# Optimization experiments

Hardware: AMD Instinct MI355X
Metric: run time of the kernel (lower is better)

The kernel has to match this reference:

```python
import jax, jax.numpy as jnp
import numpy as np

N, M = 2048, 16384          # rows = target points, cols = density-map pixels
SIGMA = 0.1                 # entropic regularization
TOL = 5e-4                  # 5 * 0.0001 convergence threshold from the source
MAX_ITERS = 100
EPS = 1e-7


def setup_inputs() -> dict:
    key = jax.random.key(0)
    k1, k2, k3 = jax.random.split(key, 3)
    dis_mtx_cross = jax.random.uniform(k1, (N, M), dtype=jnp.float32)
    pre_density = jax.random.uniform(k2, (M,), dtype=jnp.float32)
    target_mass = jax.random.uniform(k3, (N,), dtype=jnp.float32)
    return {
        "dis_mtx_cross": dis_mtx_cross,
        "pre_density": pre_density,
        "target_mass": target_mass,
    }


def _c_transform(pow_dis, alpha):
    # -log( sum_i alpha_i * exp(-pow_dis[i, :]) + eps ), reduce over dim 0
    s = jnp.sum(jnp.exp(-pow_dis) * alpha[:, None], axis=0)
    return -jnp.log(s + EPS)


def reference(dis_mtx_cross, pre_density, target_mass):
    D = dis_mtx_cross / SIGMA  # done once in __init__ in the original
    n, m = D.shape

    def step(carry, _):
        g, f, done = carry
        # one Sinkhorn c-transform sweep (runs at least once, as in torch)
        f_new = _c_transform(D - g[:, None], target_mass) / (1.0 + SIGMA)
        g_new = _c_transform(D.T - f_new[:, None], pre_density)
        diff = SIGMA * jnp.mean(jnp.abs(g_new - g))
        # freeze state once converged (emulates the torch `break`)
        g_out = jnp.where(done, g, g_new)
        f_out = jnp.where(done, f, f_new)
        done = done | (diff < TOL)
        return (g_out, f_out, done), None

    g0 = jnp.zeros((n,), jnp.float32)
    f0 = jnp.zeros((m,), jnp.float32)
    (g, f, _), _ = jax.lax.scan(step, (g0, f0, jnp.array(False)), None,
                                length=MAX_ITERS)
    g = g * SIGMA
    f = 1.0 - jnp.exp(-f * SIGMA)
    return f, g
```

## Files before the change

kernel.cpp:

```cpp
#include <hip/hip_runtime.h>
#include <math.h>

#define NN 2048
#define MM 16384

typedef __attribute__((ext_vector_type(4))) float f32x4;
typedef __attribute__((ext_vector_type(2))) float f32x2;


__global__ __launch_bounds__(256)
void k_prep(const float* __restrict__ D,
            unsigned char* __restrict__ K8,
            unsigned char* __restrict__ KT8) {
    __shared__ unsigned char t[64][72];
    const int j0 = blockIdx.x * 64, i0 = blockIdx.y * 64;
    const int tid = threadIdx.x;
    const int r = tid >> 4, c4 = tid & 15;
#pragma unroll
    for (int rp = 0; rp < 4; ++rp) {
        const int row = i0 + rp * 16 + r;
        f32x4 d = *(const f32x4*)(D + (size_t)row * MM + j0 + c4 * 4);
        float e0 = __expf(-10.0f * d[0]);
        float e1 = __expf(-10.0f * d[1]);
        float e2 = __expf(-10.0f * d[2]);
        float e3 = __expf(-10.0f * d[3]);
        int p = __builtin_amdgcn_cvt_pk_fp8_f32(e0, e1, 0, false);
        p = __builtin_amdgcn_cvt_pk_fp8_f32(e2, e3, p, true);
        *(unsigned*)(K8 + (size_t)row * MM + j0 + c4 * 4) = (unsigned)p;
        t[c4 * 4 + 0][rp * 16 + r] = (unsigned char)(p & 0xff);
        t[c4 * 4 + 1][rp * 16 + r] = (unsigned char)((p >> 8) & 0xff);
        t[c4 * 4 + 2][rp * 16 + r] = (unsigned char)((p >> 16) & 0xff);
        t[c4 * 4 + 3][rp * 16 + r] = (unsigned char)((p >> 24) & 0xff);
    }
    __syncthreads();
#pragma unroll
    for (int p2 = 0; p2 < 4; ++p2) {
        const int item = p2 * 256 + tid;
        const int jl = item >> 4, iw = item & 15;
        unsigned val = *(const unsigned*)&t[jl][iw * 4];
        *(unsigned*)(KT8 + (size_t)(j0 + jl) * NN + i0 + iw * 4) = val;
    }
}

__global__ void k_init(const float* __restrict__ tm,
                       float* __restrict__ g, float* __restrict__ w,
                       unsigned* __restrict__ counter, int* __restrict__ done) {
    const int i = blockIdx.x * 256 + threadIdx.x;
    if (i < NN) { g[i] = 0.0f; w[i] = tm[i]; }
    if (i == 0) { *counter = 0u; *done = 0; }
}

__global__ __launch_bounds__(256, 2)
void k_phaseA(const unsigned char* __restrict__ KT8, const float* __restrict__ pd,
              const float* __restrict__ w, float* __restrict__ f,
              float* __restrict__ v, const int* __restrict__ done) {
    if (*done) return;
    const int tid = threadIdx.x, lane = tid & 63, wid = tid >> 6;

    float wr[2][16];
#pragma unroll
    for (int k = 0; k < 2; ++k) {
        const f32x4* p = (const f32x4*)(w + k * 1024 + lane * 16);
#pragma unroll
        for (int q = 0; q < 4; ++q) {
            f32x4 a = p[q];
            wr[k][q * 4 + 0] = a[0]; wr[k][q * 4 + 1] = a[1];
            wr[k][q * 4 + 2] = a[2]; wr[k][q * 4 + 3] = a[3];
        }
    }
    const int jbase = blockIdx.x * 16 + wid * 4;
#pragma unroll
    for (int r = 0; r < 4; ++r) {
        const int j = jbase + r;
        const unsigned char* row = KT8 + (size_t)j * NN;
        float acc = 0.0f;
#pragma unroll
        for (int k = 0; k < 2; ++k) {
            uint4 qw = *(const uint4*)(row + k * 1024 + lane * 16);
            unsigned u[4] = {qw.x, qw.y, qw.z, qw.w};
#pragma unroll
            for (int c = 0; c < 4; ++c) {
                f32x2 lo = __builtin_amdgcn_cvt_pk_f32_fp8(u[c], false);
                f32x2 hi = __builtin_amdgcn_cvt_pk_f32_fp8(u[c], true);
                acc = fmaf(lo[0], wr[k][c * 4 + 0], acc);
                acc = fmaf(lo[1], wr[k][c * 4 + 1], acc);
                acc = fmaf(hi[0], wr[k][c * 4 + 2], acc);
                acc = fmaf(hi[1], wr[k][c * 4 + 3], acc);
            }
        }
#pragma unroll
        for (int s = 32; s; s >>= 1) acc += __shfl_xor(acc, s, 64);
        if (lane == 0) {
            float fj = -__logf(acc + 1e-7f) * (1.0f / 1.1f);
            f[j] = fj;
            v[j] = pd[j] * __expf(fj);
        }
    }
}

__global__ __launch_bounds__(256, 2)
void k_phaseB(const unsigned char* __restrict__ K8, const float* __restrict__ tm,
              const float* __restrict__ v, float* __restrict__ g,
              float* __restrict__ w, float* __restrict__ diffpart,
              unsigned* __restrict__ counter, int* __restrict__ done) {
    if (*done) return;
    const int tid = threadIdx.x;
    const int i0  = blockIdx.x * 4;

    float vr[4][16];
#pragma unroll
    for (int k = 0; k < 4; ++k) {
        const f32x4* p = (const f32x4*)(v + k * 4096 + tid * 16);
#pragma unroll
        for (int q = 0; q < 4; ++q) {
            f32x4 a = p[q];
            vr[k][q * 4 + 0] = a[0]; vr[k][q * 4 + 1] = a[1];
            vr[k][q * 4 + 2] = a[2]; vr[k][q * 4 + 3] = a[3];
        }
    }
    f32x4 accv = {0.f, 0.f, 0.f, 0.f};
#pragma unroll
    for (int r = 0; r < 4; ++r) {
        const unsigned char* row = K8 + (size_t)(i0 + r) * MM;
        float acc = 0.0f;
#pragma unroll
        for (int k = 0; k < 4; ++k) {
            uint4 qw = *(const uint4*)(row + k * 4096 + tid * 16);
            unsigned u[4] = {qw.x, qw.y, qw.z, qw.w};
#pragma unroll
            for (int c = 0; c < 4; ++c) {
                f32x2 lo = __builtin_amdgcn_cvt_pk_f32_fp8(u[c], false);
                f32x2 hi = __builtin_amdgcn_cvt_pk_f32_fp8(u[c], true);
                acc = fmaf(lo[0], vr[k][c * 4 + 0], acc);
                acc = fmaf(lo[1], vr[k][c * 4 + 1], acc);
                acc = fmaf(hi[0], vr[k][c * 4 + 2], acc);
                acc = fmaf(hi[1], vr[k][c * 4 + 3], acc);
            }
        }
        accv[r] = acc;
    }
    __shared__ f32x4 red[256];
    red[tid] = accv;
    __syncthreads();
    for (int s = 128; s; s >>= 1) {
        if (tid < s) red[tid] += red[tid + s];
        __syncthreads();
    }
    __shared__ bool last;
    if (tid == 0) {
        f32x4 sv = red[0];
        float dp = 0.0f;
#pragma unroll
        for (int r = 0; r < 4; ++r) {
            float gn = -__logf(sv[r] + 1e-7f);
            dp += fabsf(gn - g[i0 + r]);
            g[i0 + r] = gn;
            w[i0 + r] = tm[i0 + r] * __expf(gn);
        }
        diffpart[blockIdx.x] = dp;
        __threadfence();
        unsigned old = atomicAdd(counter, 1u);
        last = (old == gridDim.x - 1);
    }
    __syncthreads();

    if (last) {
        __threadfence();
        __shared__ float red1[256];
        red1[tid] = diffpart[tid] + diffpart[tid + 256];
        __syncthreads();
        for (int s2 = 128; s2; s2 >>= 1) {
            if (tid < s2) red1[tid] += red1[tid + s2];
            __syncthreads();
        }
        if (tid == 0) {
            if (0.1f * (red1[0] / (float)NN) < 5e-4f) *done = 1;
            *counter = 0u;
        }
    }
}

__global__ void k_out(const float* __restrict__ f,
                      const float* __restrict__ g,
                      float* __restrict__ out) {
    const int idx = blockIdx.x * 256 + threadIdx.x;
    if (idx < MM) {
        out[idx] = 1.0f - __expf(-0.1f * f[idx]);
    } else if (idx < MM + NN) {
        out[idx] = 0.1f * g[idx - MM];
    }
}

__global__ void k_f_partial(const float* __restrict__ dis,
                            const float* __restrict__ tm,
                            const float* __restrict__ g,
                            float* __restrict__ s_f,
                            const int* __restrict__ done) {
    if (*done) return;
    const int j  = blockIdx.x * 256 + threadIdx.x;
    const int i0 = blockIdx.y * (NN / 8);
    const float* p = dis + (size_t)i0 * MM + j;
    float acc = 0.f;
#pragma unroll 4
    for (int i = 0; i < NN / 8; ++i) {
        float d = p[(size_t)i * MM];
        float e = __expf(fmaf(d, -10.0f, g[i0 + i]));
        acc = fmaf(tm[i0 + i], e, acc);
    }
    atomicAdd(&s_f[j], acc);
}

__global__ void k_f_final(float* __restrict__ f, float* __restrict__ s_f,
                          const int* __restrict__ done) {
    if (*done) return;
    const int j = blockIdx.x * 256 + threadIdx.x;
    f[j] = -__logf(s_f[j] + 1e-7f) * (1.0f / 1.1f);
    s_f[j] = 0.f;
}

__global__ void k_g_row(const float* __restrict__ dis,
                        const float* __restrict__ pd,
                        const float* __restrict__ f,
                        float* __restrict__ g,
                        float* __restrict__ diff_acc,
                        const int* __restrict__ done) {
    if (*done) return;
    const int i = blockIdx.x;
    const float* p = dis + (size_t)i * MM;
    float acc = 0.f;
#pragma unroll 4
    for (int j = threadIdx.x; j < MM; j += 256) {
        float e = __expf(fmaf(p[j], -10.0f, f[j]));
        acc = fmaf(pd[j], e, acc);
    }
    __shared__ float red[256];
    red[threadIdx.x] = acc;
    __syncthreads();
    for (int s = 128; s > 0; s >>= 1) {
        if (threadIdx.x < s) red[threadIdx.x] += red[threadIdx.x + s];
        __syncthreads();
    }
    if (threadIdx.x == 0) {
        float gn = -__logf(red[0] + 1e-7f);
        atomicAdd(diff_acc, fabsf(gn - g[i]));
        g[i] = gn;
    }
}

__global__ void k_check(float* __restrict__ diff_acc, int* __restrict__ done) {
    if (!*done) {
        float diff = 0.1f * (*diff_acc / (float)NN);
        if (diff < 5e-4f) *done = 1;
    }
    *diff_acc = 0.f;
}

extern "C" void kernel_launch(void* const* d_in, const int* in_sizes, int n_in,
                              void* d_out, int out_size, void* d_ws, size_t ws_size,
                              hipStream_t stream) {
    const float* dis = (const float*)d_in[0];
    const float* pd  = (const float*)d_in[1];
    const float* tm  = (const float*)d_in[2];
    float* out = (float*)d_out;

    const size_t kBytes = (size_t)NN * MM;
    const size_t need   = 2 * kBytes
                        + (size_t)(2 * MM + 3 * NN + 512) * sizeof(float) + 64;

    if (ws_size >= need) {
        unsigned char* K8  = (unsigned char*)d_ws;
        unsigned char* KT8 = (unsigned char*)d_ws + kBytes;
        float* fbuf     = (float*)((char*)d_ws + 2 * kBytes);
        float* vbuf     = fbuf + MM;
        float* gbuf     = vbuf + MM;
        float* wbuf     = gbuf + NN;
        float* diffpart = wbuf + NN;
        unsigned* counter = (unsigned*)(diffpart + 512);
        int*      done    = (int*)(counter + 1);

        k_init<<<(NN + 255) / 256, 256, 0, stream>>>(tm, gbuf, wbuf, counter, done);
        k_prep<<<dim3(MM / 64, NN / 64), 256, 0, stream>>>(dis, K8, KT8);

        for (int it = 0; it < 100; ++it) {
            k_phaseA<<<1024, 256, 0, stream>>>(KT8, pd, wbuf, fbuf, vbuf, done);
            k_phaseB<<<512, 256, 0, stream>>>(K8, tm, vbuf, gbuf, wbuf,
                                              diffpart, counter, done);
        }
        k_out<<<(MM + NN + 255) / 256, 256, 0, stream>>>(fbuf, gbuf, out);
    } else {
        float* g        = (float*)d_ws;
        float* f        = g + NN;
        float* s_f      = f + MM;
        float* diff_acc = s_f + MM;
        int*   done     = (int*)(diff_acc + 1);

        hipMemsetAsync(d_ws, 0, (size_t)(NN + 2 * MM + 2) * sizeof(float), stream);

        dim3 gridF(MM / 256, 8);
        for (int it = 0; it < 100; ++it) {
            k_f_partial<<<gridF, 256, 0, stream>>>(dis, tm, g, s_f, done);
            k_f_final<<<MM / 256, 256, 0, stream>>>(f, s_f, done);
            k_g_row<<<NN, 256, 0, stream>>>(dis, pd, f, g, diff_acc, done);
            k_check<<<1, 1, 0, stream>>>(diff_acc, done);
        }
        k_out<<<(MM + NN + 255) / 256, 256, 0, stream>>>(f, g, out);
    }
}
```

Measured before the change: 909.6 us.

## Fuse Sinkhorn phases into one kernel with in-kernel grid barrier

Merges the two per-iteration kernels into a single kernel of 512 blocks. Each block computes 32 columns of f, then joins a global atomic-counter barrier before computing its rows of g. The init kernel is folded into the prep kernel. This halves the kernel launches and their gaps per iteration. In exchange it relies on all 512 blocks being co-resident, which launch_bounds(256,2) is meant to guarantee; if they are not, the spin barrier can deadlock. Phase A work per block doubles.

After: 2.106 ms. 2.32x slower.

```diff
diff --git a/kernel.cpp b/kernel.cpp
--- a/kernel.cpp
+++ b/kernel.cpp
@@ -3,15 +3,27 @@
 
 #define NN 2048
 #define MM 16384
+#define NB 512
 
 typedef __attribute__((ext_vector_type(4))) float f32x4;
 typedef __attribute__((ext_vector_type(2))) float f32x2;
+
+struct Bar { unsigned cntA; unsigned cntB; int flagA; int done; };
 
 
 __global__ __launch_bounds__(256)
 void k_prep(const float* __restrict__ D,
             unsigned char* __restrict__ K8,
-            unsigned char* __restrict__ KT8) {
+            unsigned char* __restrict__ KT8,
+            const float* __restrict__ tm,
+            float* __restrict__ g, float* __restrict__ w,
+            Bar* __restrict__ bar) {
+    if (blockIdx.x == 0 && blockIdx.y == 0) {
+        for (int i = threadIdx.x; i < NN; i += 256) { g[i] = 0.0f; w[i] = tm[i]; }
+        if (threadIdx.x == 0) {
+            bar->cntA = 0u; bar->cntB = 0u; bar->flagA = 0; bar->done = 0;
+        }
+    }
     __shared__ unsigned char t[64][72];
     const int j0 = blockIdx.x * 64, i0 = blockIdx.y * 64;
     const int tid = threadIdx.x;
@@ -42,71 +54,73 @@
     }
 }
 
-__global__ void k_init(const float* __restrict__ tm,
-                       float* __restrict__ g, float* __restrict__ w,
-                       unsigned* __restrict__ counter, int* __restrict__ done) {
-    const int i = blockIdx.x * 256 + threadIdx.x;
-    if (i < NN) { g[i] = 0.0f; w[i] = tm[i]; }
-    if (i == 0) { *counter = 0u; *done = 0; }
-}
-
 __global__ __launch_bounds__(256, 2)
-void k_phaseA(const unsigned char* __restrict__ KT8, const float* __restrict__ pd,
-              const float* __restrict__ w, float* __restrict__ f,
-              float* __restrict__ v, const int* __restrict__ done) {
-    if (*done) return;
+void k_iter(const unsigned char* __restrict__ K8,
+            const unsigned char* __restrict__ KT8,
+            const float* __restrict__ pd, const float* __restrict__ tm,
+            float* __restrict__ f, float* __restrict__ v,
+            float* __restrict__ g, float* __restrict__ w,
+            float* __restrict__ diffpart, Bar* __restrict__ bar, int it) {
+    if (bar->done) return;
     const int tid = threadIdx.x, lane = tid & 63, wid = tid >> 6;
 
-    float wr[2][16];
-#pragma unroll
-    for (int k = 0; k < 2; ++k) {
-        const f32x4* p = (const f32x4*)(w + k * 1024 + lane * 16);
-#pragma unroll
-        for (int q = 0; q < 4; ++q) {
-            f32x4 a = p[q];
-            wr[k][q * 4 + 0] = a[0]; wr[k][q * 4 + 1] = a[1];
-            wr[k][q * 4 + 2] = a[2]; wr[k][q * 4 + 3] = a[3];
-        }
-    }
-    const int jbase = blockIdx.x * 16 + wid * 4;
-#pragma unroll
-    for (int r = 0; r < 4; ++r) {
-        const int j = jbase + r;
-        const unsigned char* row = KT8 + (size_t)j * NN;
-        float acc = 0.0f;
+    {
+        float wr[2][16];
 #pragma unroll
         for (int k = 0; k < 2; ++k) {
-            uint4 qw = *(const uint4*)(row + k * 1024 + lane * 16);
-            unsigned u[4] = {qw.x, qw.y, qw.z, qw.w};
-#pragma unroll
-            for (int c = 0; c < 4; ++c) {
-                f32x2 lo = __builtin_amdgcn_cvt_pk_f32_fp8(u[c], false);
-                f32x2 hi = __builtin_amdgcn_cvt_pk_f32_fp8(u[c], true);
-                acc = fmaf(lo[0], wr[k][c * 4 + 0], acc);
-                acc = fmaf(lo[1], wr[k][c * 4 + 1], acc);
-                acc = fmaf(hi[0], wr[k][c * 4 + 2], acc);
-                acc = fmaf(hi[1], wr[k][c * 4 + 3], acc);
+            const f32x4* p = (const f32x4*)(w + k * 1024 + lane * 16);
+#pragma unroll
+            for (int q = 0; q < 4; ++q) {
+                f32x4 a = p[q];
+                wr[k][q * 4 + 0] = a[0]; wr[k][q * 4 + 1] = a[1];
+                wr[k][q * 4 + 2] = a[2]; wr[k][q * 4 + 3] = a[3];
             }
         }
-#pragma unroll
-        for (int s = 32; s; s >>= 1) acc += __shfl_xor(acc, s, 64);
-        if (lane == 0) {
-            float fj = -__logf(acc + 1e-7f) * (1.0f / 1.1f);
-            f[j] = fj;
-            v[j] = pd[j] * __expf(fj);
-        }
-    }
-}
-
-__global__ __launch_bounds__(256, 2)
-void k_phaseB(const unsigned char* __restrict__ K8, const float* __restrict__ tm,
-              const float* __restrict__ v, float* __restrict__ g,
-              float* __restrict__ w, float* __restrict__ diffpart,
-              unsigned* __restrict__ counter, int* __restrict__ done) {
-    if (*done) return;
-    const int tid = threadIdx.x;
-    const int i0  = blockIdx.x * 4;
-
+        const int jbase = blockIdx.x * 32 + wid * 8;
+#pragma unroll
+        for (int r = 0; r < 8; ++r) {
+            const int j = jbase + r;
+            const unsigned char* row = KT8 + (size_t)j * NN;
+            float acc = 0.0f;
+#pragma unroll
+            for (int k = 0; k < 2; ++k) {
+                uint4 qw = *(const uint4*)(row + k * 1024 + lane * 16);
+                unsigned u[4] = {qw.x, qw.y, qw.z, qw.w};
+#pragma unroll
+                for (int c = 0; c < 4; ++c) {
+                    f32x2 lo = __builtin_amdgcn_cvt_pk_f32_fp8(u[c], false);
+                    f32x2 hi = __builtin_amdgcn_cvt_pk_f32_fp8(u[c], true);
+                    acc = fmaf(lo[0], wr[k][c * 4 + 0], acc);
+                    acc = fmaf(lo[1], wr[k][c * 4 + 1], acc);
+                    acc = fmaf(hi[0], wr[k][c * 4 + 2], acc);
+                    acc = fmaf(hi[1], wr[k][c * 4 + 3], acc);
+                }
+            }
+#pragma unroll
+            for (int s = 32; s; s >>= 1) acc += __shfl_xor(acc, s, 64);
+            if (lane == 0) {
+                float fj = -__logf(acc + 1e-7f) * (1.0f / 1.1f);
+                f[j] = fj;
+                v[j] = pd[j] * __expf(fj);
+            }
+        }
+    }
+
+    __syncthreads();
+    if (tid == 0) {
+        __threadfence();
+        unsigned old = atomicAdd(&bar->cntA, 1u);
+        if (old == (unsigned)(NB * it + NB - 1))
+            __hip_atomic_store(&bar->flagA, it + 1, __ATOMIC_RELEASE,
+                               __HIP_MEMORY_SCOPE_AGENT);
+        while (__hip_atomic_load(&bar->flagA, __ATOMIC_ACQUIRE,
+                                 __HIP_MEMORY_SCOPE_AGENT) < it + 1)
+            __builtin_amdgcn_s_sleep(1);
+        __threadfence();
+    }
+    __syncthreads();
+
+    const int i0 = blockIdx.x * 4;
     float vr[4][16];
 #pragma unroll
     for (int k = 0; k < 4; ++k) {
@@ -159,24 +173,22 @@
         }
         diffpart[blockIdx.x] = dp;
         __threadfence();
-        unsigned old = atomicAdd(counter, 1u);
-        last = (old == gridDim.x - 1);
+        unsigned old = atomicAdd(&bar->cntB, 1u);
+        last = (old == (unsigned)(NB * it + NB - 1));
     }
     __syncthreads();
 
     if (last) {
         __threadfence();
-        __shared__ float red1[256];
-        red1[tid] = diffpart[tid] + diffpart[tid + 256];
+        __shared__ float redc[256];
+        redc[tid] = diffpart[tid] + diffpart[tid + 256];
         __syncthreads();
         for (int s2 = 128; s2; s2 >>= 1) {
-            if (tid < s2) red1[tid] += red1[tid + s2];
+            if (tid < s2) redc[tid] += redc[tid + s2];
             __syncthreads();
         }
-        if (tid == 0) {
-            if (0.1f * (red1[0] / (float)NN) < 5e-4f) *done = 1;
-            *counter = 0u;
-        }
+        if (tid == 0 && 0.1f * (redc[0] / (float)NN) < 5e-4f)
+            bar->done = 1;
     }
 }
 
@@ -265,7 +277,7 @@
 
     const size_t kBytes = (size_t)NN * MM;
     const size_t need   = 2 * kBytes
-                        + (size_t)(2 * MM + 3 * NN + 512) * sizeof(float) + 64;
+                        + (size_t)(2 * MM + 2 * NN + NB) * sizeof(float) + 64;
 
     if (ws_size >= need) {
         unsigned char* K8  = (unsigned char*)d_ws;
@@ -275,16 +287,13 @@
         float* gbuf     = vbuf + MM;
         float* wbuf     = gbuf + NN;
         float* diffpart = wbuf + NN;
-        unsigned* counter = (unsigned*)(diffpart + 512);
-        int*      done    = (int*)(counter + 1);
-
-        k_init<<<(NN + 255) / 256, 256, 0, stream>>>(tm, gbuf, wbuf, counter, done);
-        k_prep<<<dim3(MM / 64, NN / 64), 256, 0, stream>>>(dis, K8, KT8);
-
+        Bar*   bar      = (Bar*)(diffpart + NB);
+
+        k_prep<<<dim3(MM / 64, NN / 64), 256, 0, stream>>>(dis, K8, KT8,
+                                                           tm, gbuf, wbuf, bar);
         for (int it = 0; it < 100; ++it) {
-            k_phaseA<<<1024, 256, 0, stream>>>(KT8, pd, wbuf, fbuf, vbuf, done);
-            k_phaseB<<<512, 256, 0, stream>>>(K8, tm, vbuf, gbuf, wbuf,
-                                              diffpart, counter, done);
+            k_iter<<<NB, 256, 0, stream>>>(K8, KT8, pd, tm, fbuf, vbuf,
+                                           gbuf, wbuf, diffpart, bar, it);
         }
         k_out<<<(MM + NN + 255) / 256, 256, 0, stream>>>(fbuf, gbuf, out);
     } else {
```
